# Kernel tuning notes

Measured on AMD Instinct MI355X. Metric: run time of the kernel, lower is better.

## Reference

```python
import jax, jax.numpy as jnp
import numpy as np

S, I = 512, 384
C_MSA, C_Z, H, C = 64, 128, 8, 32
EPS = 1e-5


def _layernorm(x, g, b):
    mu = jnp.mean(x, axis=-1, keepdims=True)
    var = jnp.var(x, axis=-1, keepdims=True)
    return (x - mu) * jax.lax.rsqrt(var + EPS) * g + b


def setup_inputs() -> dict:
    key = jax.random.key(0)
    ks = jax.random.split(key, 6)
    sc_v = 1.0 / np.sqrt(C_MSA)
    sc_z = 1.0 / np.sqrt(C_Z)
    sc_o = 1.0 / np.sqrt(H * C)
    return {
        "msa_SI": jax.random.normal(ks[0], (S, I, C_MSA), jnp.float32),
        "pair_II": jax.random.normal(ks[1], (I, I, C_Z), jnp.float32),
        "ln_msa_g": jnp.ones((C_MSA,), jnp.float32),
        "ln_msa_b": jnp.zeros((C_MSA,), jnp.float32),
        "ln_pair_g": jnp.ones((C_Z,), jnp.float32),
        "ln_pair_b": jnp.zeros((C_Z,), jnp.float32),
        "W_v": jax.random.normal(ks[2], (C_MSA, H * C), jnp.float32) * sc_v,
        "W_bias": jax.random.normal(ks[3], (C_Z, H), jnp.float32) * sc_z,
        "W_gate": jax.random.normal(ks[4], (C_MSA, H * C), jnp.float32) * sc_v,
        "W_out": jax.random.normal(ks[5], (H * C, C_MSA), jnp.float32) * sc_o,
    }


def reference(msa_SI, pair_II, ln_msa_g, ln_msa_b, ln_pair_g, ln_pair_b,
              W_v, W_bias, W_gate, W_out):
    s, i = msa_SI.shape[:2]
    msa_n = _layernorm(msa_SI, ln_msa_g, ln_msa_b)              # [S,I,Cm]
    v_SIHC = (msa_n @ W_v).reshape(s, i, H, C)                   # [S,I,H,C]
    bias_IIH = _layernorm(pair_II, ln_pair_g, ln_pair_b) @ W_bias  # [I,I,H]
    w_IIH = jax.nn.softmax(bias_IIH, axis=-2)                    # softmax over j
    gate = jax.nn.sigmoid(msa_n @ W_gate)                        # [S,I,H*C]
    # weighted average shared across S: [I,I,H] x [S,I,H,C] -> [S,I,H,C]
    weights = jnp.einsum('ijh,sjhc->sihc', w_IIH, v_SIHC).reshape(s, i, H * C)
    o = gate * weights
    return o @ W_out                                             # [S,I,Cm]
```

## Files before the change

### kernel.cpp

```cpp
#include <hip/hip_runtime.h>
#include <hip/hip_bf16.h>

#define S_DIM 512
#define I_DIM 384
#define CM 64
#define CZ 128
#define H_DIM 8
#define C_DIM 32
#define HC 256
#define II (I_DIM*I_DIM)

typedef short bf16x8 __attribute__((ext_vector_type(8)));
typedef float f32x4 __attribute__((ext_vector_type(4)));

__device__ __forceinline__ float s2f(short s) {
    unsigned int u = ((unsigned int)(unsigned short)s) << 16;
    float f; __builtin_memcpy(&f, &u, 4); return f;
}
__device__ __forceinline__ short f2bf(float f) {
    __hip_bfloat16 h = __float2bfloat16(f);
    short r; __builtin_memcpy(&r, &h, 2); return r;
}

__device__ __forceinline__ void glds16(const short* g, short* l) {
    __builtin_amdgcn_global_load_lds(
        (const __attribute__((address_space(1))) void*)g,
        (__attribute__((address_space(3))) void*)l, 16, 0, 0);
}

__global__ __launch_bounds__(256) void k_pair_ln_bias(
    const float* __restrict__ pair, const float* __restrict__ g,
    const float* __restrict__ b, const float* __restrict__ Wb,
    float* __restrict__ bias)
{
    __shared__ float xs[4][CZ];
    __shared__ float WbT[H_DIM*132];
    const int tid = threadIdx.x;
    const int wv = tid >> 6, lane = tid & 63;
    const int ij = blockIdx.x*4 + wv;

    {
        float4 q = *(const float4*)(Wb + tid*4);
        int m = tid*4;
        WbT[(m&7)*132 + (m>>3)]     = q.x;
        WbT[((m+1)&7)*132 + ((m+1)>>3)] = q.y;
        WbT[((m+2)&7)*132 + ((m+2)>>3)] = q.z;
        WbT[((m+3)&7)*132 + ((m+3)>>3)] = q.w;
    }

    float2 x2 = *(const float2*)(pair + (size_t)ij*CZ + lane*2);
    float s1 = x2.x + x2.y;
    float s2 = x2.x*x2.x + x2.y*x2.y;
#pragma unroll
    for (int off = 32; off > 0; off >>= 1) {
        s1 += __shfl_xor(s1, off, 64);
        s2 += __shfl_xor(s2, off, 64);
    }
    float mu = s1 * (1.f/CZ);
    float var = s2 * (1.f/CZ) - mu*mu;
    float rs = rsqrtf(var + 1e-5f);
    xs[wv][lane*2]   = (x2.x - mu)*rs*g[lane*2]   + b[lane*2];
    xs[wv][lane*2+1] = (x2.y - mu)*rs*g[lane*2+1] + b[lane*2+1];
    __syncthreads();

    const int h = lane >> 3, seg = lane & 7;
    float p = 0.f;
#pragma unroll
    for (int jj = 0; jj < 16; jj++) {
        int c = seg + jj*8;
        p += xs[wv][c] * WbT[h*132 + c];
    }
    p += __shfl_down(p, 4, 64);
    p += __shfl_down(p, 2, 64);
    p += __shfl_down(p, 1, 64);
    if (seg == 0) bias[(size_t)h*II + ij] = p;
}

__global__ __launch_bounds__(384) void k_softmax(
    const float* __restrict__ bias, short* __restrict__ w)
{
    int blk = blockIdx.x;
    int i = blk >> 3, h = blk & 7;
    int j = threadIdx.x;
    float x = bias[(size_t)h*II + i*I_DIM + j];
    float m = x;
#pragma unroll
    for (int off = 32; off > 0; off >>= 1) m = fmaxf(m, __shfl_xor(m, off, 64));
    __shared__ float red[6];
    int wv = j >> 6;
    if ((j & 63) == 0) red[wv] = m;
    __syncthreads();
    m = red[0];
#pragma unroll
    for (int k = 1; k < 6; k++) m = fmaxf(m, red[k]);
    float e = __expf(x - m);
    float s = e;
#pragma unroll
    for (int off = 32; off > 0; off >>= 1) s += __shfl_xor(s, off, 64);
    __syncthreads();
    if ((j & 63) == 0) red[wv] = s;
    __syncthreads();
    s = 0.f;
#pragma unroll
    for (int k = 0; k < 6; k++) s += red[k];
    w[(size_t)h*II + i*I_DIM + j] = f2bf(e / s);
}

__global__ __launch_bounds__(256) void k_prep_w(
    const float* __restrict__ Wv, const float* __restrict__ Wg,
    const float* __restrict__ Wo,
    short* __restrict__ Wt, short* __restrict__ Wot)
{
    int idx = blockIdx.x*256 + threadIdx.x;
    if (idx < 512*64) {
        int n = idx >> 6, k = idx & 63;
        Wt[idx] = f2bf((n < HC) ? Wv[k*HC + n] : Wg[k*HC + (n - HC)]);
    } else {
        int q = idx - 512*64;
        int n = q >> 8, k = q & 255;
        Wot[q] = f2bf(Wo[k*64 + n]);
    }
}

__global__ __launch_bounds__(256) void k4_ln_vgate(
    const float* __restrict__ msa_c,
    const float* __restrict__ gm, const float* __restrict__ bm,
    const short* __restrict__ Wt,
    short* __restrict__ v_t, short* __restrict__ gate)
{
    __shared__ alignas(16) short lds[20992];
    short* As = lds;
    short* Bs = lds + 4608;
    short* T  = lds;

    const int tid = threadIdx.x;
    const int wave = tid >> 6;
    const int lane = tid & 63;
    const int pm = blockIdx.y;

    {
        const int row = tid >> 2;
        const int seg = tid & 3;
        float xf[16], gf[16], bf[16];
        const float* rp = msa_c + (size_t)(pm*64 + row)*CM + seg*16;
#pragma unroll
        for (int q = 0; q < 4; q++) {
            float4 a = *(const float4*)(rp + q*4);
            xf[q*4] = a.x; xf[q*4+1] = a.y; xf[q*4+2] = a.z; xf[q*4+3] = a.w;
            float4 gg = *(const float4*)(gm + seg*16 + q*4);
            gf[q*4] = gg.x; gf[q*4+1] = gg.y; gf[q*4+2] = gg.z; gf[q*4+3] = gg.w;
            float4 bb = *(const float4*)(bm + seg*16 + q*4);
            bf[q*4] = bb.x; bf[q*4+1] = bb.y; bf[q*4+2] = bb.z; bf[q*4+3] = bb.w;
        }
        float s1 = 0.f, s2 = 0.f;
#pragma unroll
        for (int j = 0; j < 16; j++) { s1 += xf[j]; s2 += xf[j]*xf[j]; }
        s1 += __shfl_xor(s1, 1); s2 += __shfl_xor(s2, 1);
        s1 += __shfl_xor(s1, 2); s2 += __shfl_xor(s2, 2);
        float mu = s1 * (1.f/64.f);
        float var = s2 * (1.f/64.f) - mu*mu;
        float rs = rsqrtf(var + 1e-5f);
        bf16x8 o0, o1;
#pragma unroll
        for (int j = 0; j < 8; j++) {
            o0[j] = f2bf((xf[j]   - mu)*rs*gf[j]   + bf[j]);
            o1[j] = f2bf((xf[8+j] - mu)*rs*gf[8+j] + bf[8+j]);
        }
        *(bf16x8*)&As[row*72 + seg*16]     = o0;
        *(bf16x8*)&As[row*72 + seg*16 + 8] = o1;
    }

    const int lr = lane >> 2, lq = lane & 3;
    const int fr = lane & 15, fq = lane >> 4;
    f32x4 acc[4][8] = {};

    for (int kt = 0; kt < 2; ++kt) {
#pragma unroll
        for (int c2 = 0; c2 < 8; c2++) {
            int ch = wave + c2*4;
            glds16(Wt + (ch*16 + lr)*64 + kt*32 + lq*8, &Bs[ch*512]);
        }
        __syncthreads();

        bf16x8 af[4], bfrag[8];
#pragma unroll
        for (int mi = 0; mi < 4; mi++)
            af[mi] = *(const bf16x8*)&As[(mi*16 + fr)*72 + kt*32 + fq*8];
#pragma unroll
        for (int ni = 0; ni < 8; ni++)
            bfrag[ni] = *(const bf16x8*)&Bs[(wave*128 + ni*16 + fr)*32 + fq*8];
#pragma unroll
        for (int mi = 0; mi < 4; mi++)
#pragma unroll
            for (int ni = 0; ni < 8; ni++)
                acc[mi][ni] = __builtin_amdgcn_mfma_f32_16x16x32_bf16(
                    af[mi], bfrag[ni], acc[mi][ni], 0, 0, 0);
        __syncthreads();
    }

    const int s_local = pm / 6;
    const int j0 = (pm % 6) * 64;
    if (wave < 2) {
#pragma unroll
        for (int mi = 0; mi < 4; mi++)
#pragma unroll
        for (int ni = 0; ni < 8; ni++) {
            int cl = wave*128 + ni*16 + fr;
            short4 pk;
            pk.x = f2bf(acc[mi][ni][0]);
            pk.y = f2bf(acc[mi][ni][1]);
            pk.z = f2bf(acc[mi][ni][2]);
            pk.w = f2bf(acc[mi][ni][3]);
            *(short4*)&T[cl*72 + mi*16 + fq*4] = pk;
        }
    } else {
#pragma unroll
        for (int mi = 0; mi < 4; mi++)
#pragma unroll
        for (int ni = 0; ni < 8; ni++)
#pragma unroll
        for (int r = 0; r < 4; r++) {
            int rowg = pm*64 + mi*16 + fq*4 + r;
            int col = (wave - 2)*128 + ni*16 + fr;
            gate[(size_t)rowg*HC + col] =
                f2bf(1.f/(1.f + __expf(-acc[mi][ni][r])));
        }
    }
    __syncthreads();
#pragma unroll
    for (int p = 0; p < 8; p++) {
        int unit = p*256 + tid;
        int cl = unit >> 3, part = unit & 7;
        bf16x8 d = *(const bf16x8*)&T[cl*72 + part*8];
        int h = cl >> 5, cc = cl & 31;
        *(bf16x8*)&v_t[(((size_t)s_local*H_DIM + h)*C_DIM + cc)*I_DIM + j0 + part*8] = d;
    }
}

__global__ __launch_bounds__(256, 2) void k56_einsum_proj(
    const short* __restrict__ w,
    const short* __restrict__ v_t,
    const short* __restrict__ gate,
    const short* __restrict__ Wot,
    float* __restrict__ out)
{
    __shared__ alignas(16) short Ws[384*32];
    __shared__ alignas(16) short Vs[32*32];
    __shared__ alignas(16) short Ob[384*40];
    const int tid = threadIdx.x;
    const int wave = tid >> 6, lane = tid & 63;
    const int lr = lane >> 2, lq = lane & 3;
    const int fr = lane & 15, fq = lane >> 4;
    const int s = blockIdx.x;

    f32x4 acc_o[6][4] = {};

    for (int h = 0; h < H_DIM; h++) {
        bf16x8 bw[4];
#pragma unroll
        for (int ni = 0; ni < 4; ni++)
            bw[ni] = *(const bf16x8*)&Wot[(ni*16 + fr)*HC + h*C_DIM + fq*8];

        f32x4 acc_e[2][6] = {};
        const short* wb = w + (size_t)h*II;
        const short* vb = v_t + (((size_t)s*H_DIM + h)*C_DIM)*I_DIM;
        for (int kt = 0; kt < 12; kt++) {
#pragma unroll
            for (int c2 = 0; c2 < 6; c2++) {
                int ch = wave + c2*4;
                glds16(wb + (ch*16 + lr)*I_DIM + kt*32 + lq*8, &Ws[ch*512]);
            }
            if (wave < 2)
                glds16(vb + (wave*16 + lr)*I_DIM + kt*32 + lq*8, &Vs[wave*512]);
            __syncthreads();

            bf16x8 av[2], bwv[6];
#pragma unroll
            for (int mi = 0; mi < 2; mi++)
                av[mi] = *(const bf16x8*)&Vs[(mi*16 + fr)*32 + fq*8];
#pragma unroll
            for (int ni = 0; ni < 6; ni++)
                bwv[ni] = *(const bf16x8*)&Ws[(wave*96 + ni*16 + fr)*32 + fq*8];
#pragma unroll
            for (int mi = 0; mi < 2; mi++)
#pragma unroll
                for (int ni = 0; ni < 6; ni++)
                    acc_e[mi][ni] = __builtin_amdgcn_mfma_f32_16x16x32_bf16(
                        av[mi], bwv[ni], acc_e[mi][ni], 0, 0, 0);
            __syncthreads();
        }

#pragma unroll
        for (int mi = 0; mi < 2; mi++)
#pragma unroll
        for (int ni = 0; ni < 6; ni++) {
            int i = wave*96 + ni*16 + fr;
            int c0 = mi*16 + fq*4;
            short4 gv = *(const short4*)&gate[(size_t)(s*I_DIM + i)*HC + h*C_DIM + c0];
            short4 pk;
            pk.x = f2bf(acc_e[mi][ni][0] * s2f(gv.x));
            pk.y = f2bf(acc_e[mi][ni][1] * s2f(gv.y));
            pk.z = f2bf(acc_e[mi][ni][2] * s2f(gv.z));
            pk.w = f2bf(acc_e[mi][ni][3] * s2f(gv.w));
            *(short4*)&Ob[i*40 + c0] = pk;
        }
        __syncthreads();

        bf16x8 ao[6];
#pragma unroll
        for (int mi = 0; mi < 6; mi++)
            ao[mi] = *(const bf16x8*)&Ob[(wave*96 + mi*16 + fr)*40 + fq*8];
#pragma unroll
        for (int mi = 0; mi < 6; mi++)
#pragma unroll
            for (int ni = 0; ni < 4; ni++)
                acc_o[mi][ni] = __builtin_amdgcn_mfma_f32_16x16x32_bf16(
                    ao[mi], bw[ni], acc_o[mi][ni], 0, 0, 0);
    }

#pragma unroll
    for (int mi = 0; mi < 6; mi++)
#pragma unroll
    for (int ni = 0; ni < 4; ni++)
#pragma unroll
    for (int r = 0; r < 4; r++) {
        int i = wave*96 + mi*16 + fq*4 + r;
        int n = ni*16 + fr;
        out[(size_t)(s*I_DIM + i)*CM + n] = acc_o[mi][ni][r];
    }
}

extern "C" void kernel_launch(void* const* d_in, const int* in_sizes, int n_in,
                              void* d_out, int out_size, void* d_ws, size_t ws_size,
                              hipStream_t stream)
{
    const float* msa  = (const float*)d_in[0];
    const float* pair = (const float*)d_in[1];
    const float* gm   = (const float*)d_in[2];
    const float* bm   = (const float*)d_in[3];
    const float* gp   = (const float*)d_in[4];
    const float* bp   = (const float*)d_in[5];
    const float* Wv   = (const float*)d_in[6];
    const float* Wb   = (const float*)d_in[7];
    const float* Wg   = (const float*)d_in[8];
    const float* Wo   = (const float*)d_in[9];

    char* ws = (char*)d_ws;
    short* w    = (short*)ws;
    short* Wt   = (short*)(ws + 2359296);
    short* Wot  = (short*)(ws + 2424832);
    char*  region = ws + 2457600;
    float* bias = (float*)region;

    size_t avail = (ws_size > 2457600u) ? (ws_size - 2457600u) : 0;
    int Sc = 8;
    const int scs[7] = {512, 256, 128, 64, 32, 16, 8};
    for (int i = 0; i < 7; i++) {
        size_t need = (size_t)scs[i] * 393216u;
        if (need < 4718592u) need = 4718592u;
        if (need <= avail) { Sc = scs[i]; break; }
    }
    const int NC = S_DIM / Sc;
    short* v_t  = (short*)region;
    short* gate = (short*)(region + (size_t)Sc*196608u);

    k_pair_ln_bias<<<dim3(II/4), dim3(256), 0, stream>>>(pair, gp, bp, Wb, bias);
    k_prep_w<<<dim3(192), dim3(256), 0, stream>>>(Wv, Wg, Wo, Wt, Wot);
    k_softmax<<<dim3(I_DIM*H_DIM), dim3(I_DIM), 0, stream>>>(bias, w);

    for (int c = 0; c < NC; c++) {
        size_t in_off = (size_t)c * Sc * I_DIM * CM;

        k4_ln_vgate<<<dim3(1, Sc*6, 1), dim3(256), 0, stream>>>(
            msa + in_off, gm, bm, Wt, v_t, gate);

        k56_einsum_proj<<<dim3(Sc), dim3(256), 0, stream>>>(
            w, v_t, gate, Wot, (float*)d_out + in_off);
    }
}
```

Before: 432.5 us.

## Split einsum-projection kernel over i halves and double-buffer LDS tiles

The einsum+projection kernel now launches two blocks per sequence row, each covering 192 of the 384 i rows, which halves per-block registers and LDS and raises the occupancy target to 3 blocks. The W/V tile loads are double-buffered so the next k-tile (including the first tile of the next head) is staged while MFMAs run, with one barrier per iteration instead of two. Gate and Wot loads are hoisted into the loop to hide their latency. The cost is that each v tile is loaded twice, once per half, and there is extra bookkeeping.

```diff
diff --git a/kernel.cpp b/kernel.cpp
--- a/kernel.cpp
+++ b/kernel.cpp
@@ -237,94 +237,119 @@
     }
 }
 
-__global__ __launch_bounds__(256, 2) void k56_einsum_proj(
+__global__ __launch_bounds__(256, 3) void k56_einsum_proj(
     const short* __restrict__ w,
     const short* __restrict__ v_t,
     const short* __restrict__ gate,
     const short* __restrict__ Wot,
     float* __restrict__ out)
 {
-    __shared__ alignas(16) short Ws[384*32];
-    __shared__ alignas(16) short Vs[32*32];
-    __shared__ alignas(16) short Ob[384*40];
+    __shared__ alignas(16) short Ws[2][192*32];
+    __shared__ alignas(16) short Vs[2][32*32];
+    __shared__ alignas(16) short Ob[192*40];
     const int tid = threadIdx.x;
     const int wave = tid >> 6, lane = tid & 63;
     const int lr = lane >> 2, lq = lane & 3;
     const int fr = lane & 15, fq = lane >> 4;
-    const int s = blockIdx.x;
-
-    f32x4 acc_o[6][4] = {};
+    const int ih = blockIdx.x;
+    const int s  = blockIdx.y;
+    const int ibase = ih*192;
+
+    f32x4 acc_o[3][4] = {};
+
+    const short* wb = w;
+    const short* vb = v_t + (size_t)s*H_DIM*C_DIM*I_DIM;
+
+    auto stage = [&](const short* wb_, const short* vb_, int kt_, int buf) {
+#pragma unroll
+        for (int c2 = 0; c2 < 3; c2++) {
+            int ch = wave + c2*4;
+            glds16(wb_ + (size_t)(ibase + ch*16 + lr)*I_DIM + kt_*32 + lq*8,
+                   &Ws[buf][ch*512]);
+        }
+        if (wave < 2)
+            glds16(vb_ + (size_t)(wave*16 + lr)*I_DIM + kt_*32 + lq*8,
+                   &Vs[buf][wave*512]);
+    };
+
+    stage(wb, vb, 0, 0);
 
     for (int h = 0; h < H_DIM; h++) {
+        const short* wb_n = wb + II;
+        const short* vb_n = vb + C_DIM*I_DIM;
+        f32x4 acc_e[2][3] = {};
+        short4 gv[2][3];
         bf16x8 bw[4];
 #pragma unroll
-        for (int ni = 0; ni < 4; ni++)
-            bw[ni] = *(const bf16x8*)&Wot[(ni*16 + fr)*HC + h*C_DIM + fq*8];
-
-        f32x4 acc_e[2][6] = {};
-        const short* wb = w + (size_t)h*II;
-        const short* vb = v_t + (((size_t)s*H_DIM + h)*C_DIM)*I_DIM;
         for (int kt = 0; kt < 12; kt++) {
-#pragma unroll
-            for (int c2 = 0; c2 < 6; c2++) {
-                int ch = wave + c2*4;
-                glds16(wb + (ch*16 + lr)*I_DIM + kt*32 + lq*8, &Ws[ch*512]);
+            __syncthreads();
+            if (kt < 11)      stage(wb, vb, kt+1, (kt+1)&1);
+            else if (h < 7)   stage(wb_n, vb_n, 0, 0);
+            if (kt == 10) {
+#pragma unroll
+                for (int ni = 0; ni < 4; ni++)
+                    bw[ni] = *(const bf16x8*)&Wot[(ni*16 + fr)*HC + h*C_DIM + fq*8];
+#pragma unroll
+                for (int mi = 0; mi < 2; mi++)
+#pragma unroll
+                for (int ni = 0; ni < 3; ni++) {
+                    int i = ibase + wave*48 + ni*16 + fr;
+                    gv[mi][ni] = *(const short4*)&gate[
+                        (size_t)(s*I_DIM + i)*HC + h*C_DIM + mi*16 + fq*4];
+                }
             }
-            if (wave < 2)
-                glds16(vb + (wave*16 + lr)*I_DIM + kt*32 + lq*8, &Vs[wave*512]);
-            __syncthreads();
-
-            bf16x8 av[2], bwv[6];
+            const int cb = kt & 1;
+            bf16x8 av[2], bwv[3];
 #pragma unroll
             for (int mi = 0; mi < 2; mi++)
-                av[mi] = *(const bf16x8*)&Vs[(mi*16 + fr)*32 + fq*8];
-#pragma unroll
-            for (int ni = 0; ni < 6; ni++)
-                bwv[ni] = *(const bf16x8*)&Ws[(wave*96 + ni*16 + fr)*32 + fq*8];
+                av[mi] = *(const bf16x8*)&Vs[cb][(mi*16 + fr)*32 + fq*8];
+#pragma unroll
+            for (int ni = 0; ni < 3; ni++)
+                bwv[ni] = *(const bf16x8*)&Ws[cb][(wave*48 + ni*16 + fr)*32 + fq*8];
 #pragma unroll
             for (int mi = 0; mi < 2; mi++)
 #pragma unroll
-                for (int ni = 0; ni < 6; ni++)
+                for (int ni = 0; ni < 3; ni++)
                     acc_e[mi][ni] = __builtin_amdgcn_mfma_f32_16x16x32_bf16(
                         av[mi], bwv[ni], acc_e[mi][ni], 0, 0, 0);
-            __syncthreads();
         }
 
 #pragma unroll
         for (int mi = 0; mi < 2; mi++)
 #pragma unroll
-        for (int ni = 0; ni < 6; ni++) {
-            int i = wave*96 + ni*16 + fr;
+        for (int ni = 0; ni < 3; ni++) {
+            int il = wave*48 + ni*16 + fr;
             int c0 = mi*16 + fq*4;
-            short4 gv = *(const short4*)&gate[(size_t)(s*I_DIM + i)*HC + h*C_DIM + c0];
+            short4 g = gv[mi][ni];
             short4 pk;
-            pk.x = f2bf(acc_e[mi][ni][0] * s2f(gv.x));
-            pk.y = f2bf(acc_e[mi][ni][1] * s2f(gv.y));
-            pk.z = f2bf(acc_e[mi][ni][2] * s2f(gv.z));
-            pk.w = f2bf(acc_e[mi][ni][3] * s2f(gv.w));
-            *(short4*)&Ob[i*40 + c0] = pk;
+            pk.x = f2bf(acc_e[mi][ni][0] * s2f(g.x));
+            pk.y = f2bf(acc_e[mi][ni][1] * s2f(g.y));
+            pk.z = f2bf(acc_e[mi][ni][2] * s2f(g.z));
+            pk.w = f2bf(acc_e[mi][ni][3] * s2f(g.w));
+            *(short4*)&Ob[il*40 + c0] = pk;
         }
         __syncthreads();
 
-        bf16x8 ao[6];
-#pragma unroll
-        for (int mi = 0; mi < 6; mi++)
-            ao[mi] = *(const bf16x8*)&Ob[(wave*96 + mi*16 + fr)*40 + fq*8];
-#pragma unroll
-        for (int mi = 0; mi < 6; mi++)
+        bf16x8 ao[3];
+#pragma unroll
+        for (int mi = 0; mi < 3; mi++)
+            ao[mi] = *(const bf16x8*)&Ob[(wave*48 + mi*16 + fr)*40 + fq*8];
+#pragma unroll
+        for (int mi = 0; mi < 3; mi++)
 #pragma unroll
             for (int ni = 0; ni < 4; ni++)
                 acc_o[mi][ni] = __builtin_amdgcn_mfma_f32_16x16x32_bf16(
                     ao[mi], bw[ni], acc_o[mi][ni], 0, 0, 0);
-    }
-
-#pragma unroll
-    for (int mi = 0; mi < 6; mi++)
+        wb = wb_n; vb = vb_n;
+    }
+
+#pragma unroll
+    for (int mi = 0; mi < 3; mi++)
 #pragma unroll
     for (int ni = 0; ni < 4; ni++)
 #pragma unroll
     for (int r = 0; r < 4; r++) {
-        int i = wave*96 + mi*16 + fq*4 + r;
+        int i = ibase + wave*48 + mi*16 + fq*4 + r;
         int n = ni*16 + fr;
         out[(size_t)(s*I_DIM + i)*CM + n] = acc_o[mi][ni][r];
     }
@@ -374,7 +399,7 @@
         k4_ln_vgate<<<dim3(1, Sc*6, 1), dim3(256), 0, stream>>>(
             msa + in_off, gm, bm, Wt, v_t, gate);
 
-        k56_einsum_proj<<<dim3(Sc), dim3(256), 0, stream>>>(
+        k56_einsum_proj<<<dim3(2, Sc), dim3(256), 0, stream>>>(
             w, v_t, gate, Wot, (float*)d_out + in_off);
     }
 }
```

Result: slower. 446.1 us (+3.1%).

## Double-buffer einsum staging, split blocks over i-halves and s-pairs, prefetch gate

Applied to the files above, without the earlier changes.

The einsum/projection kernel now double-buffers the softmax-weight and V tiles in LDS with explicit vmcnt waits, so loads for step kt+2 overlap the MFMAs of step kt. It also changes work decomposition: each block handles 192 rows of i for two s values, so the W tile is shared across two sequences and each wave gets a private output buffer, which removes a block-wide barrier. Gate and W_out fragments are prefetched early, and MFMA sections get raised priority. The LN/vgate kernel issues its first B-tile load before the layernorm and prefetches the second tile after the first MFMA pass, using a transposed LDS layout. Costs are more LDS, more hand-tuned waitcnt logic, and an assumption that Sc is even.

```diff
diff --git a/kernel.cpp b/kernel.cpp
--- a/kernel.cpp
+++ b/kernel.cpp
@@ -138,6 +138,14 @@
     const int lane = tid & 63;
     const int pm = blockIdx.y;
 
+    auto stage_b = [&](int kt) {
+#pragma unroll
+        for (int c2 = 0; c2 < 8; c2++)
+            glds16(Wt + (size_t)(c2*64 + lane)*64 + kt*32 + wave*8,
+                   &Bs[(wave*512 + c2*64)*8]);
+    };
+    stage_b(0);
+
     {
         const int row = tid >> 2;
         const int seg = tid & 3;
@@ -170,16 +178,10 @@
         *(bf16x8*)&As[row*72 + seg*16 + 8] = o1;
     }
 
-    const int lr = lane >> 2, lq = lane & 3;
     const int fr = lane & 15, fq = lane >> 4;
     f32x4 acc[4][8] = {};
 
     for (int kt = 0; kt < 2; ++kt) {
-#pragma unroll
-        for (int c2 = 0; c2 < 8; c2++) {
-            int ch = wave + c2*4;
-            glds16(Wt + (ch*16 + lr)*64 + kt*32 + lq*8, &Bs[ch*512]);
-        }
         __syncthreads();
 
         bf16x8 af[4], bfrag[8];
@@ -188,7 +190,7 @@
             af[mi] = *(const bf16x8*)&As[(mi*16 + fr)*72 + kt*32 + fq*8];
 #pragma unroll
         for (int ni = 0; ni < 8; ni++)
-            bfrag[ni] = *(const bf16x8*)&Bs[(wave*128 + ni*16 + fr)*32 + fq*8];
+            bfrag[ni] = *(const bf16x8*)&Bs[(fq*512 + wave*128 + ni*16 + fr)*8];
 #pragma unroll
         for (int mi = 0; mi < 4; mi++)
 #pragma unroll
@@ -196,6 +198,7 @@
                 acc[mi][ni] = __builtin_amdgcn_mfma_f32_16x16x32_bf16(
                     af[mi], bfrag[ni], acc[mi][ni], 0, 0, 0);
         __syncthreads();
+        if (kt == 0) stage_b(1);
     }
 
     const int s_local = pm / 6;
@@ -244,78 +247,111 @@
     const short* __restrict__ Wot,
     float* __restrict__ out)
 {
-    __shared__ alignas(16) short Ws[384*32];
-    __shared__ alignas(16) short Vs[32*32];
-    __shared__ alignas(16) short Ob[384*40];
+    __shared__ alignas(16) short Ws[2][4*192*8];
+    __shared__ alignas(16) short Vs[2][2][1024];
+    __shared__ alignas(16) short Ob[4][96*40];
     const int tid = threadIdx.x;
     const int wave = tid >> 6, lane = tid & 63;
-    const int lr = lane >> 2, lq = lane & 3;
     const int fr = lane & 15, fq = lane >> 4;
-    const int s = blockIdx.x;
+    const int ibase = blockIdx.x * 192;
+    const int sp = blockIdx.y;
+    const int ms = wave >> 1;
+    const int kv = wave & 1;
+    const int s  = sp*2 + ms;
+    const int iw = kv * 96;
+
+    const short* vbm = v_t + (size_t)s * H_DIM * C_DIM * I_DIM;
+
+    auto stage = [&](int h_, int kt_, int buf) {
+        const short* wp = w + (size_t)h_*II + kt_*32 + wave*8;
+#pragma unroll
+        for (int rg = 0; rg < 3; rg++)
+            glds16(wp + (size_t)(ibase + rg*64 + lane)*I_DIM,
+                   &Ws[buf][(wave*192 + rg*64)*8]);
+        glds16(vbm + (size_t)h_*C_DIM*I_DIM + (lane & 31)*I_DIM + kt_*32
+                   + (2*kv + (lane >> 5))*8,
+               &Vs[buf][ms][kv*512]);
+    };
 
     f32x4 acc_o[6][4] = {};
 
+    stage(0, 0, 0);
+    stage(0, 1, 1);
+
     for (int h = 0; h < H_DIM; h++) {
+        f32x4 acc_e[2][6] = {};
+        short4 gv[2][6];
         bf16x8 bw[4];
 #pragma unroll
-        for (int ni = 0; ni < 4; ni++)
-            bw[ni] = *(const bf16x8*)&Wot[(ni*16 + fr)*HC + h*C_DIM + fq*8];
-
-        f32x4 acc_e[2][6] = {};
-        const short* wb = w + (size_t)h*II;
-        const short* vb = v_t + (((size_t)s*H_DIM + h)*C_DIM)*I_DIM;
         for (int kt = 0; kt < 12; kt++) {
-#pragma unroll
-            for (int c2 = 0; c2 < 6; c2++) {
-                int ch = wave + c2*4;
-                glds16(wb + (ch*16 + lr)*I_DIM + kt*32 + lq*8, &Ws[ch*512]);
+            const int cb = kt & 1;
+            asm volatile("s_waitcnt vmcnt(4)" ::: "memory");
+            __builtin_amdgcn_s_barrier();
+            __builtin_amdgcn_sched_barrier(0);
+
+            bf16x8 av[2], bwv[6];
+#pragma unroll
+            for (int mi = 0; mi < 2; mi++)
+                av[mi] = *(const bf16x8*)&Vs[cb][ms][(fq*32 + mi*16 + fr)*8];
+#pragma unroll
+            for (int ni = 0; ni < 6; ni++)
+                bwv[ni] = *(const bf16x8*)&Ws[cb][(fq*192 + iw + ni*16 + fr)*8];
+            asm volatile("s_waitcnt lgkmcnt(0)" ::: "memory");
+            __builtin_amdgcn_s_barrier();
+            __builtin_amdgcn_sched_barrier(0);
+
+            if (kt == 10) {
+#pragma unroll
+                for (int ni = 0; ni < 4; ni++)
+                    bw[ni] = *(const bf16x8*)&Wot[(ni*16 + fr)*HC + h*C_DIM + fq*8];
+#pragma unroll
+                for (int mi = 0; mi < 2; mi++)
+#pragma unroll
+                for (int ni = 0; ni < 6; ni++)
+                    gv[mi][ni] = *(const short4*)&gate[
+                        (size_t)(s*I_DIM + ibase + iw + ni*16 + fr)*HC
+                        + h*C_DIM + mi*16 + fq*4];
             }
-            if (wave < 2)
-                glds16(vb + (wave*16 + lr)*I_DIM + kt*32 + lq*8, &Vs[wave*512]);
-            __syncthreads();
-
-            bf16x8 av[2], bwv[6];
-#pragma unroll
-            for (int mi = 0; mi < 2; mi++)
-                av[mi] = *(const bf16x8*)&Vs[(mi*16 + fr)*32 + fq*8];
-#pragma unroll
-            for (int ni = 0; ni < 6; ni++)
-                bwv[ni] = *(const bf16x8*)&Ws[(wave*96 + ni*16 + fr)*32 + fq*8];
+            if (kt < 10)          stage(h, kt + 2, cb);
+            else if (h < 7)       stage(h + 1, kt - 10, cb);
+
+            __builtin_amdgcn_s_setprio(1);
 #pragma unroll
             for (int mi = 0; mi < 2; mi++)
 #pragma unroll
                 for (int ni = 0; ni < 6; ni++)
                     acc_e[mi][ni] = __builtin_amdgcn_mfma_f32_16x16x32_bf16(
                         av[mi], bwv[ni], acc_e[mi][ni], 0, 0, 0);
-            __syncthreads();
-        }
-
+            __builtin_amdgcn_s_setprio(0);
+        }
+
+        short* myOb = Ob[wave];
 #pragma unroll
         for (int mi = 0; mi < 2; mi++)
 #pragma unroll
         for (int ni = 0; ni < 6; ni++) {
-            int i = wave*96 + ni*16 + fr;
+            int row = ni*16 + fr;
             int c0 = mi*16 + fq*4;
-            short4 gv = *(const short4*)&gate[(size_t)(s*I_DIM + i)*HC + h*C_DIM + c0];
+            short4 g = gv[mi][ni];
             short4 pk;
-            pk.x = f2bf(acc_e[mi][ni][0] * s2f(gv.x));
-            pk.y = f2bf(acc_e[mi][ni][1] * s2f(gv.y));
-            pk.z = f2bf(acc_e[mi][ni][2] * s2f(gv.z));
-            pk.w = f2bf(acc_e[mi][ni][3] * s2f(gv.w));
-            *(short4*)&Ob[i*40 + c0] = pk;
-        }
-        __syncthreads();
-
+            pk.x = f2bf(acc_e[mi][ni][0] * s2f(g.x));
+            pk.y = f2bf(acc_e[mi][ni][1] * s2f(g.y));
+            pk.z = f2bf(acc_e[mi][ni][2] * s2f(g.z));
+            pk.w = f2bf(acc_e[mi][ni][3] * s2f(g.w));
+            *(short4*)&myOb[row*40 + c0] = pk;
+        }
         bf16x8 ao[6];
 #pragma unroll
         for (int mi = 0; mi < 6; mi++)
-            ao[mi] = *(const bf16x8*)&Ob[(wave*96 + mi*16 + fr)*40 + fq*8];
+            ao[mi] = *(const bf16x8*)&myOb[(mi*16 + fr)*40 + fq*8];
+        __builtin_amdgcn_s_setprio(1);
 #pragma unroll
         for (int mi = 0; mi < 6; mi++)
 #pragma unroll
             for (int ni = 0; ni < 4; ni++)
                 acc_o[mi][ni] = __builtin_amdgcn_mfma_f32_16x16x32_bf16(
                     ao[mi], bw[ni], acc_o[mi][ni], 0, 0, 0);
+        __builtin_amdgcn_s_setprio(0);
     }
 
 #pragma unroll
@@ -324,7 +360,7 @@
     for (int ni = 0; ni < 4; ni++)
 #pragma unroll
     for (int r = 0; r < 4; r++) {
-        int i = wave*96 + mi*16 + fq*4 + r;
+        int i = ibase + iw + mi*16 + fq*4 + r;
         int n = ni*16 + fr;
         out[(size_t)(s*I_DIM + i)*CM + n] = acc_o[mi][ni][r];
     }
@@ -374,7 +410,7 @@
         k4_ln_vgate<<<dim3(1, Sc*6, 1), dim3(256), 0, stream>>>(
             msa + in_off, gm, bm, Wt, v_t, gate);
 
-        k56_einsum_proj<<<dim3(Sc), dim3(256), 0, stream>>>(
+        k56_einsum_proj<<<dim3(2, Sc/2), dim3(256), 0, stream>>>(
             w, v_t, gate, Wot, (float*)d_out + in_off);
     }
 }
```

Result: slower. 460.5 us (+6.5%).
